# Performance work log

Hardware: AMD Instinct MI355X
Metric: run time of the kernel (lower is better)

The kernel has to match this reference:

```python
import jax, jax.numpy as jnp
import numpy as np

IMAGE_SIZE = 1024
DOWNSIZING = 64
THRESHOLD = 0.65  # default_threshold_target (threshold arg == 0)
NUM_BG_POINTS = 1
ORI_SHAPE = (2160, 3840)
EMBED_C, FEAT_H, FEAT_W = 256, 64, 64


def setup_inputs() -> dict:
    key = jax.random.key(0)
    k1, k2 = jax.random.split(key)
    image_embeddings = jax.random.normal(k1, (1, EMBED_C, FEAT_H, FEAT_W), dtype=jnp.float32)
    reference_feat = jax.random.normal(k2, (1, EMBED_C), dtype=jnp.float32) * 0.1
    ori_shape = jnp.array(ORI_SHAPE, dtype=jnp.int32)
    return {"image_embeddings": image_embeddings, "reference_feat": reference_feat, "ori_shape": ori_shape}


def _postprocess_masks(sim, H, W):
    # F.interpolate to (image_size, image_size), crop to pre-padded size, resize to ori_shape
    sim = jax.image.resize(sim, (1, 1, IMAGE_SIZE, IMAGE_SIZE), method="bilinear", antialias=False)
    scale = IMAGE_SIZE / max(H, W)
    ph = int(np.floor(H * scale + 0.5))
    pw = int(np.floor(W * scale + 0.5))
    sim = sim[..., :ph, :pw]
    return jax.image.resize(sim, (1, 1, H, W), method="bilinear", antialias=False)


def reference(image_embeddings, reference_feat, ori_shape):
    H, W = int(ori_shape[0]), int(ori_shape[1])
    # --- similarity map ---
    t = image_embeddings[0]                                   # (C, hf, wf)
    c, hf, wf = t.shape
    t = t / jnp.linalg.norm(t, axis=0, keepdims=True)         # channel-wise L2 norm
    sim = (reference_feat @ t.reshape(c, hf * wf)).reshape(1, 1, hf, wf)
    sim = _postprocess_masks(sim, H, W)
    m = sim[0, 0]                                             # (H, W)
    flat = m.reshape(-1)                                      # (H*W,)
    hw = H * W

    # --- background points: k smallest values ---
    _, bg_idx = jax.lax.top_k(-flat, NUM_BG_POINTS)
    bg_row = bg_idx // W
    bg_col = bg_idx % W
    bg_coords = jnp.stack([bg_col, bg_row], axis=1).astype(jnp.float32)  # (N, 2) = (x, y)

    # --- foreground points: grid-binned per-cell max (segment-max form of
    #     torch.where + unique + broadcast-equality + per-bin topk) ---
    ratio = IMAGE_SIZE / max(H, W)
    n_cells_side = IMAGE_SIZE // DOWNSIZING                    # 16; bounds grid rows/cols
    num_cells = n_cells_side * n_cells_side                    # 256 fixed
    idx = jnp.arange(hw, dtype=jnp.int32)
    ys = idx // W
    xs = idx % W
    gy = jnp.floor(ys * (ratio / DOWNSIZING)).astype(jnp.int32)
    gx = jnp.floor(xs * (ratio / DOWNSIZING)).astype(jnp.int32)
    seg = gy * n_cells_side + gx                               # grid id per pixel

    valid = flat > THRESHOLD
    masked = jnp.where(valid, flat, -jnp.inf)
    seg_max = jax.ops.segment_max(masked, seg, num_segments=num_cells)
    # first pixel achieving the cell max (matches torch.topk tie behavior)
    is_max = valid & (masked == seg_max[seg])
    cand = jnp.where(is_max, idx, hw)
    best = jax.ops.segment_min(cand, seg, num_segments=num_cells)
    cell_valid = best < hw
    bi = jnp.minimum(best, hw - 1)
    px = (bi % W).astype(jnp.float32)
    py = (bi // W).astype(jnp.float32)
    ps = flat[bi]
    points = jnp.stack([px, py, ps], axis=1)                   # (num_cells, 3) = (x, y, score)
    points = jnp.where(cell_valid[:, None], points, -1.0)      # mimic F.pad(value=-1) rows
    sort_key = jnp.where(cell_valid, ps, -jnp.inf)
    order = jnp.argsort(-sort_key)                             # score descending, invalid last
    points_scores = points[order]
    return points_scores, bg_coords
```

## Files before the change

### kernel.cpp

```cpp
#include <hip/hip_runtime.h>

#define W_OUT 3840
#define H_OUT 2160
#define IW 1024
#define IH 576
#define BAND 240

__device__ __forceinline__ unsigned int enc_f32(float f) {
    unsigned int b = __float_as_uint(f);
    return b ^ (0x80000000u | (unsigned int)((int)b >> 31));
}

__device__ __forceinline__ void release_vmem() {
    asm volatile("s_waitcnt vmcnt(0)" ::: "memory");
}

__global__ __launch_bounds__(256) void sim_kernel(
    const float* __restrict__ emb, const float* __restrict__ ref,
    float* __restrict__ sim,
    unsigned int* __restrict__ bandCnt,
    unsigned int* __restrict__ doneCnt)
{
    if (blockIdx.x == 0) {
        const int t = threadIdx.x;
        if (t < 9)          bandCnt[t * 16] = 0u;
        else if (t == 9)    *doneCnt = 0u;
    }
    const int lane = threadIdx.x & 63;
    const int wave = threadIdx.x >> 6;
    const int p = blockIdx.x * 64 + lane;
    const int cbase = wave * 64;
    float dot = 0.f, ss = 0.f;
#pragma unroll 8
    for (int cc = 0; cc < 64; ++cc) {
        int c = cbase + cc;
        float a = emb[c * 4096 + p];
        dot = fmaf(ref[c], a, dot);
        ss  = fmaf(a, a, ss);
    }
    __shared__ float sdot[4][64];
    __shared__ float sss[4][64];
    sdot[wave][lane] = dot;
    sss[wave][lane]  = ss;
    __syncthreads();
    if (wave == 0) {
        float d = (sdot[0][lane] + sdot[1][lane]) + (sdot[2][lane] + sdot[3][lane]);
        float s = (sss[0][lane] + sss[1][lane]) + (sss[2][lane] + sss[3][lane]);
        sim[p] = d / sqrtf(s);
    }
}

__global__ __launch_bounds__(256) void scan_kernel(
    const float* __restrict__ sim,
    unsigned long long* __restrict__ cellPart,
    unsigned long long* __restrict__ bgPart,
    unsigned long long* __restrict__ bandTab,
    unsigned long long* __restrict__ bgBand,
    unsigned int* __restrict__ bandCnt,
    unsigned int* __restrict__ doneCnt,
    float* __restrict__ out)
{
    __shared__ float4 I4[2][IW / 4];
    __shared__ unsigned long long wmin[4];
    __shared__ unsigned long long bred[16][17];
    __shared__ unsigned int lastFlag;
    __shared__ float sk[256];
    float* I0 = (float*)&I4[0][0];
    float* I1 = (float*)&I4[1][0];

    const float INV375 = (float)(1.0 / 3.75);
    const float INV16  = 0.0625f;

    const int y   = blockIdx.x;
    const int tid = threadIdx.x;
    const int band = y / BAND;

    float fy  = ((float)y + 0.5f) * INV375 - 0.5f;
    float fyf = floorf(fy);
    float wy  = fy - fyf;
    int ai = (int)fyf;
    int a1 = min(max(ai + 1, 0), IH - 1);
    int a0 = min(max(ai,     0), IH - 1);

    for (int r = 0; r < 2; ++r) {
        int a = (r == 0) ? a0 : a1;
        float fa  = ((float)a + 0.5f) * INV16 - 0.5f;
        float faf = floorf(fa);
        float wa  = fa - faf;
        int si = (int)faf;
        int s1 = min(max(si + 1, 0), 63);
        int s0 = min(max(si,     0), 63);
        const float* row0 = sim + s0 * 64;
        const float* row1 = sim + s1 * 64;
        float* dst = (r == 0) ? I0 : I1;
        for (int b = tid; b < IW; b += 256) {
            float fb  = ((float)b + 0.5f) * INV16 - 0.5f;
            float fbf = floorf(fb);
            float wb  = fb - fbf;
            int ci = (int)fbf;
            int c1 = min(max(ci + 1, 0), 63);
            int c0 = min(max(ci,     0), 63);
            float v0 = row0[c0] * (1.f - wb) + row0[c1] * wb;
            float v1 = row1[c0] * (1.f - wb) + row1[c1] * wb;
            dst[b] = v0 * (1.f - wa) + v1 * wa;
        }
    }
    __syncthreads();

    unsigned long long bestCell = 0ull;
    unsigned long long bestBg   = 0xFFFFFFFFFFFFFFFFull;
    const int x0 = tid * 15;
    const unsigned int idxBase = (unsigned int)(y * W_OUT + x0);

#define UPD(F, jj) {                                                        \
        unsigned long long top = ((unsigned long long)enc_f32(F)) << 32;    \
        unsigned int idx = idxBase + (jj);                                  \
        unsigned long long bgk = top | (unsigned long long)idx;             \
        unsigned long long ck  = top | (unsigned long long)(~idx);          \
        if (ck  > bestCell) bestCell = ck;                                  \
        if (bgk < bestBg)   bestBg   = bgk;                                 \
    }

    if (tid == 0 || tid == 255) {
#pragma unroll
        for (int j = 0; j < 15; ++j) {
            int x = x0 + j;
            float fx  = ((float)x + 0.5f) * INV375 - 0.5f;
            float fxf = floorf(fx);
            float wx  = fx - fxf;
            int bi = (int)fxf;
            int b1 = min(max(bi + 1, 0), IW - 1);
            int b0 = min(max(bi,     0), IW - 1);
            float v0 = I0[b0] * (1.f - wx) + I0[b1] * wx;
            float v1 = I1[b0] * (1.f - wx) + I1[b1] * wx;
            float F  = v0 * (1.f - wy) + v1 * wy;
            UPD(F, j)
        }
    } else {
        float4 A0 = I4[0][tid - 1], B0 = I4[0][tid], C0 = I4[0][tid + 1];
        float4 A1 = I4[1][tid - 1], B1 = I4[1][tid], C1 = I4[1][tid + 1];
        const float rr0[12] = {A0.x,A0.y,A0.z,A0.w, B0.x,B0.y,B0.z,B0.w, C0.x,C0.y,C0.z,C0.w};
        const float rr1[12] = {A1.x,A1.y,A1.z,A1.w, B1.x,B1.y,B1.z,B1.w, C1.x,C1.y,C1.z,C1.w};

#define PX(j, i0) {                                                         \
            float fx  = ((float)(x0 + (j)) + 0.5f) * INV375 - 0.5f;         \
            float fxf = floorf(fx);                                         \
            float wx  = fx - fxf;                                           \
            float v0 = rr0[(i0)] * (1.f - wx) + rr0[(i0) + 1] * wx;         \
            float v1 = rr1[(i0)] * (1.f - wx) + rr1[(i0) + 1] * wx;         \
            float F  = v0 * (1.f - wy) + v1 * wy;                           \
            UPD(F, j)                                                       \
        }
        PX(0,3)  PX(1,3)  PX(2,4)  PX(3,4)  PX(4,4)
        PX(5,4)  PX(6,5)  PX(7,5)  PX(8,5)  PX(9,6)
        PX(10,6) PX(11,6) PX(12,6) PX(13,7) PX(14,7)
#undef PX
    }
#undef UPD

#pragma unroll
    for (int m = 1; m <= 8; m <<= 1) {
        unsigned long long o = __shfl_xor(bestCell, m, 64);
        if (o > bestCell) bestCell = o;
    }
    if ((tid & 15) == 0)
        atomicExch(&cellPart[y * 16 + (tid >> 4)], bestCell);

#pragma unroll
    for (int m = 1; m <= 32; m <<= 1) {
        unsigned long long o = __shfl_xor(bestBg, m, 64);
        if (o < bestBg) bestBg = o;
    }
    if ((tid & 63) == 0) wmin[tid >> 6] = bestBg;
    __syncthreads();
    if (tid == 0) {
        unsigned long long b0 = wmin[0] < wmin[1] ? wmin[0] : wmin[1];
        unsigned long long b1 = wmin[2] < wmin[3] ? wmin[2] : wmin[3];
        atomicExch(&bgPart[y], b0 < b1 ? b0 : b1);
        release_vmem();
        unsigned int old = atomicAdd(&bandCnt[band * 16], 1u);
        lastFlag = (old == (unsigned int)(BAND - 1)) ? 1u : 0u;
    }
    __syncthreads();
    if (!lastFlag) return;

    {
        const int cx  = tid & 15;
        const int sub = tid >> 4;
        unsigned long long* src = cellPart + (band * BAND) * 16 + cx;
        unsigned long long mx = 0ull;
#pragma unroll
        for (int i = 0; i < 15; ++i) {
            unsigned long long v = atomicMax(&src[(sub * 15 + i) * 16], 0ull);
            if (v > mx) mx = v;
        }
        bred[sub][cx] = mx;

        unsigned long long bm = (tid < BAND)
            ? atomicMin(&bgPart[band * BAND + tid], 0xFFFFFFFFFFFFFFFFull)
            : 0xFFFFFFFFFFFFFFFFull;
#pragma unroll
        for (int m = 1; m <= 32; m <<= 1) {
            unsigned long long o = __shfl_xor(bm, m, 64);
            if (o < bm) bm = o;
        }
        if ((tid & 63) == 0) wmin[tid >> 6] = bm;
    }
    __syncthreads();
    if (tid < 16) {
        unsigned long long mx = bred[0][tid];
#pragma unroll
        for (int s = 1; s < 16; ++s) {
            unsigned long long v = bred[s][tid];
            if (v > mx) mx = v;
        }
        atomicExch(&bandTab[band * 16 + tid], mx);
    }
    if (tid == 0) {
        unsigned long long b0 = wmin[0] < wmin[1] ? wmin[0] : wmin[1];
        unsigned long long b1 = wmin[2] < wmin[3] ? wmin[2] : wmin[3];
        atomicExch(&bgBand[band], b0 < b1 ? b0 : b1);
    }
    __syncthreads();
    if (tid == 0) {
        release_vmem();
        unsigned int old = atomicAdd(doneCnt, 1u);
        lastFlag = (old == 8u) ? 1u : 0u;
    }
    __syncthreads();
    if (!lastFlag) return;

    float px = -1.f, py = -1.f, ps = -1.f;
    float key = -__builtin_huge_valf();
    if (tid < 144) {
        unsigned long long best = atomicMax(&bandTab[tid], 0ull);
        if (best != 0ull) {
            unsigned int e = (unsigned int)(best >> 32);
            unsigned int b = (e & 0x80000000u) ? (e ^ 0x80000000u) : ~e;
            float v = __uint_as_float(b);
            if (v > 0.65f) {
                unsigned int idx = ~((unsigned int)(best & 0xFFFFFFFFull));
                px = (float)(idx % W_OUT);
                py = (float)(idx / W_OUT);
                ps = v;
                key = v;
            }
        }
    }

    sk[tid] = key;
    __syncthreads();
    int rank = 0;
    for (int j = 0; j < 256; ++j) {
        float kj = sk[j];
        if (kj > key || (kj == key && j < tid)) rank++;
    }
    out[rank * 3 + 0] = px;
    out[rank * 3 + 1] = py;
    out[rank * 3 + 2] = ps;

    if (tid < 16) {
        unsigned long long b = (tid < 9) ? atomicMin(&bgBand[tid], 0xFFFFFFFFFFFFFFFFull)
                                         : 0xFFFFFFFFFFFFFFFFull;
#pragma unroll
        for (int m = 1; m <= 8; m <<= 1) {
            unsigned long long o = __shfl_xor(b, m, 64);
            if (o < b) b = o;
        }
        if (tid == 0) {
            unsigned int idx = (unsigned int)(b & 0xFFFFFFFFull);
            out[256 * 3 + 0] = (float)(idx % W_OUT);
            out[256 * 3 + 1] = (float)(idx / W_OUT);
        }
    }
}

extern "C" void kernel_launch(void* const* d_in, const int* in_sizes, int n_in,
                              void* d_out, int out_size, void* d_ws, size_t ws_size,
                              hipStream_t stream) {
    (void)in_sizes; (void)n_in; (void)out_size; (void)ws_size;
    const float* emb = (const float*)d_in[0];
    const float* ref = (const float*)d_in[1];
    float* out = (float*)d_out;

    char* ws = (char*)d_ws;
    float*              sim      = (float*)ws;
    unsigned long long* cellPart = (unsigned long long*)(ws + 16384);
    unsigned long long* bgPart   = (unsigned long long*)(ws + 292864);
    unsigned long long* bandTab  = (unsigned long long*)(ws + 310144);
    unsigned long long* bgBand   = (unsigned long long*)(ws + 311296);
    unsigned int*       bandCnt  = (unsigned int*)(ws + 311424);
    unsigned int*       doneCnt  = (unsigned int*)(ws + 312000);

    sim_kernel<<<64, 256, 0, stream>>>(emb, ref, sim, bandCnt, doneCnt);
    scan_kernel<<<H_OUT, 256, 0, stream>>>(sim, cellPart, bgPart, bandTab, bgBand,
                                           bandCnt, doneCnt, out);
}
```

Baseline: 91.12 us.

## Process four output rows per scan block sharing three intermediate rows

Each scan block now handles four consecutive output rows. It builds three vertically interpolated intermediate rows in shared memory once and reuses them across the four rows, instead of building two rows per output row. This cuts the block count, the per-block reduction and atomic traffic, and the band-finalisation work. The cost is fewer blocks for parallelism and longer serial work per block.

```diff
diff --git a/kernel.cpp b/kernel.cpp
--- a/kernel.cpp
+++ b/kernel.cpp
@@ -5,6 +5,9 @@
 #define IW 1024
 #define IH 576
 #define BAND 240
+#define RPB 4
+#define NBLK (H_OUT / RPB)
+#define BPB (BAND / RPB)
 
 __device__ __forceinline__ unsigned int enc_f32(float f) {
     unsigned int b = __float_as_uint(f);
@@ -60,49 +63,47 @@
     unsigned int* __restrict__ doneCnt,
     float* __restrict__ out)
 {
-    __shared__ float4 I4[2][IW / 4];
+    __shared__ float4 IC4[3][IW / 4];
     __shared__ unsigned long long wmin[4];
     __shared__ unsigned long long bred[16][17];
     __shared__ unsigned int lastFlag;
     __shared__ float sk[256];
-    float* I0 = (float*)&I4[0][0];
-    float* I1 = (float*)&I4[1][0];
 
     const float INV375 = (float)(1.0 / 3.75);
     const float INV16  = 0.0625f;
 
-    const int y   = blockIdx.x;
+    const int blk = blockIdx.x;
+    const int y0  = blk * RPB;
     const int tid = threadIdx.x;
-    const int band = y / BAND;
-
-    float fy  = ((float)y + 0.5f) * INV375 - 0.5f;
-    float fyf = floorf(fy);
-    float wy  = fy - fyf;
-    int ai = (int)fyf;
-    int a1 = min(max(ai + 1, 0), IH - 1);
-    int a0 = min(max(ai,     0), IH - 1);
-
-    for (int r = 0; r < 2; ++r) {
-        int a = (r == 0) ? a0 : a1;
-        float fa  = ((float)a + 0.5f) * INV16 - 0.5f;
-        float faf = floorf(fa);
-        float wa  = fa - faf;
-        int si = (int)faf;
-        int s1 = min(max(si + 1, 0), 63);
-        int s0 = min(max(si,     0), 63);
-        const float* row0 = sim + s0 * 64;
-        const float* row1 = sim + s1 * 64;
-        float* dst = (r == 0) ? I0 : I1;
-        for (int b = tid; b < IW; b += 256) {
-            float fb  = ((float)b + 0.5f) * INV16 - 0.5f;
-            float fbf = floorf(fb);
-            float wb  = fb - fbf;
-            int ci = (int)fbf;
-            int c1 = min(max(ci + 1, 0), 63);
-            int c0 = min(max(ci,     0), 63);
-            float v0 = row0[c0] * (1.f - wb) + row0[c1] * wb;
-            float v1 = row1[c0] * (1.f - wb) + row1[c1] * wb;
-            dst[b] = v0 * (1.f - wa) + v1 * wa;
+    const int band = y0 / BAND;
+
+    {
+        float fy0  = ((float)y0 + 0.5f) * INV375 - 0.5f;
+        int ai0 = (int)floorf(fy0);
+        int amin = min(max(ai0, 0), IH - 1);
+
+        for (int k = 0; k < 3; ++k) {
+            int a = amin + k;
+            float fa  = ((float)a + 0.5f) * INV16 - 0.5f;
+            float faf = floorf(fa);
+            float wa  = fa - faf;
+            int si = (int)faf;
+            int s1 = min(max(si + 1, 0), 63);
+            int s0 = min(max(si,     0), 63);
+            const float* row0 = sim + s0 * 64;
+            const float* row1 = sim + s1 * 64;
+            float* dst = (float*)&IC4[k][0];
+            for (int b = tid; b < IW; b += 256) {
+                float fb  = ((float)b + 0.5f) * INV16 - 0.5f;
+                float fbf = floorf(fb);
+                float wb  = fb - fbf;
+                int ci = (int)fbf;
+                int c1 = min(max(ci + 1, 0), 63);
+                int c0 = min(max(ci,     0), 63);
+                float v0 = row0[c0] * (1.f - wb) + row0[c1] * wb;
+                float v1 = row1[c0] * (1.f - wb) + row1[c1] * wb;
+                dst[b] = v0 * (1.f - wa) + v1 * wa;
+            }
         }
     }
     __syncthreads();
@@ -110,7 +111,12 @@
     unsigned long long bestCell = 0ull;
     unsigned long long bestBg   = 0xFFFFFFFFFFFFFFFFull;
     const int x0 = tid * 15;
-    const unsigned int idxBase = (unsigned int)(y * W_OUT + x0);
+
+    int amin;
+    {
+        float fy0 = ((float)y0 + 0.5f) * INV375 - 0.5f;
+        amin = min(max((int)floorf(fy0), 0), IH - 1);
+    }
 
 #define UPD(F, jj) {                                                        \
         unsigned long long top = ((unsigned long long)enc_f32(F)) << 32;    \
@@ -121,40 +127,56 @@
         if (bgk < bestBg)   bestBg   = bgk;                                 \
     }
 
-    if (tid == 0 || tid == 255) {
-#pragma unroll
-        for (int j = 0; j < 15; ++j) {
-            int x = x0 + j;
-            float fx  = ((float)x + 0.5f) * INV375 - 0.5f;
-            float fxf = floorf(fx);
-            float wx  = fx - fxf;
-            int bi = (int)fxf;
-            int b1 = min(max(bi + 1, 0), IW - 1);
-            int b0 = min(max(bi,     0), IW - 1);
-            float v0 = I0[b0] * (1.f - wx) + I0[b1] * wx;
-            float v1 = I1[b0] * (1.f - wx) + I1[b1] * wx;
-            float F  = v0 * (1.f - wy) + v1 * wy;
-            UPD(F, j)
-        }
-    } else {
-        float4 A0 = I4[0][tid - 1], B0 = I4[0][tid], C0 = I4[0][tid + 1];
-        float4 A1 = I4[1][tid - 1], B1 = I4[1][tid], C1 = I4[1][tid + 1];
-        const float rr0[12] = {A0.x,A0.y,A0.z,A0.w, B0.x,B0.y,B0.z,B0.w, C0.x,C0.y,C0.z,C0.w};
-        const float rr1[12] = {A1.x,A1.y,A1.z,A1.w, B1.x,B1.y,B1.z,B1.w, C1.x,C1.y,C1.z,C1.w};
-
-#define PX(j, i0) {                                                         \
+#pragma unroll 1
+    for (int jr = 0; jr < RPB; ++jr) {
+        const int y = y0 + jr;
+        float fy  = ((float)y + 0.5f) * INV375 - 0.5f;
+        float fyf = floorf(fy);
+        float wy  = fy - fyf;
+        int ai = (int)fyf;
+        int a1 = min(max(ai + 1, 0), IH - 1);
+        int a0 = min(max(ai,     0), IH - 1);
+        const int i0 = a0 - amin;
+        const int i1 = a1 - amin;
+        const float* I0 = (const float*)&IC4[i0][0];
+        const float* I1 = (const float*)&IC4[i1][0];
+        const unsigned int idxBase = (unsigned int)(y * W_OUT + x0);
+
+        if (tid == 0 || tid == 255) {
+#pragma unroll
+            for (int j = 0; j < 15; ++j) {
+                int x = x0 + j;
+                float fx  = ((float)x + 0.5f) * INV375 - 0.5f;
+                float fxf = floorf(fx);
+                float wx  = fx - fxf;
+                int bi = (int)fxf;
+                int b1 = min(max(bi + 1, 0), IW - 1);
+                int b0 = min(max(bi,     0), IW - 1);
+                float v0 = I0[b0] * (1.f - wx) + I0[b1] * wx;
+                float v1 = I1[b0] * (1.f - wx) + I1[b1] * wx;
+                float F  = v0 * (1.f - wy) + v1 * wy;
+                UPD(F, j)
+            }
+        } else {
+            float4 A0 = IC4[i0][tid - 1], B0 = IC4[i0][tid], C0 = IC4[i0][tid + 1];
+            float4 A1 = IC4[i1][tid - 1], B1 = IC4[i1][tid], C1 = IC4[i1][tid + 1];
+            const float rr0[12] = {A0.x,A0.y,A0.z,A0.w, B0.x,B0.y,B0.z,B0.w, C0.x,C0.y,C0.z,C0.w};
+            const float rr1[12] = {A1.x,A1.y,A1.z,A1.w, B1.x,B1.y,B1.z,B1.w, C1.x,C1.y,C1.z,C1.w};
+
+#define PX(j, i0w) {                                                        \
             float fx  = ((float)(x0 + (j)) + 0.5f) * INV375 - 0.5f;         \
             float fxf = floorf(fx);                                         \
             float wx  = fx - fxf;                                           \
-            float v0 = rr0[(i0)] * (1.f - wx) + rr0[(i0) + 1] * wx;         \
-            float v1 = rr1[(i0)] * (1.f - wx) + rr1[(i0) + 1] * wx;         \
+            float v0 = rr0[(i0w)] * (1.f - wx) + rr0[(i0w) + 1] * wx;       \
+            float v1 = rr1[(i0w)] * (1.f - wx) + rr1[(i0w) + 1] * wx;       \
             float F  = v0 * (1.f - wy) + v1 * wy;                           \
             UPD(F, j)                                                       \
         }
-        PX(0,3)  PX(1,3)  PX(2,4)  PX(3,4)  PX(4,4)
-        PX(5,4)  PX(6,5)  PX(7,5)  PX(8,5)  PX(9,6)
-        PX(10,6) PX(11,6) PX(12,6) PX(13,7) PX(14,7)
+            PX(0,3)  PX(1,3)  PX(2,4)  PX(3,4)  PX(4,4)
+            PX(5,4)  PX(6,5)  PX(7,5)  PX(8,5)  PX(9,6)
+            PX(10,6) PX(11,6) PX(12,6) PX(13,7) PX(14,7)
 #undef PX
+        }
     }
 #undef UPD
 
@@ -164,7 +186,7 @@
         if (o > bestCell) bestCell = o;
     }
     if ((tid & 15) == 0)
-        atomicExch(&cellPart[y * 16 + (tid >> 4)], bestCell);
+        atomicExch(&cellPart[blk * 16 + (tid >> 4)], bestCell);
 
 #pragma unroll
     for (int m = 1; m <= 32; m <<= 1) {
@@ -176,10 +198,10 @@
     if (tid == 0) {
         unsigned long long b0 = wmin[0] < wmin[1] ? wmin[0] : wmin[1];
         unsigned long long b1 = wmin[2] < wmin[3] ? wmin[2] : wmin[3];
-        atomicExch(&bgPart[y], b0 < b1 ? b0 : b1);
+        atomicExch(&bgPart[blk], b0 < b1 ? b0 : b1);
         release_vmem();
         unsigned int old = atomicAdd(&bandCnt[band * 16], 1u);
-        lastFlag = (old == (unsigned int)(BAND - 1)) ? 1u : 0u;
+        lastFlag = (old == (unsigned int)(BPB - 1)) ? 1u : 0u;
     }
     __syncthreads();
     if (!lastFlag) return;
@@ -187,17 +209,20 @@
     {
         const int cx  = tid & 15;
         const int sub = tid >> 4;
-        unsigned long long* src = cellPart + (band * BAND) * 16 + cx;
+        unsigned long long* src = cellPart + (band * BPB) * 16 + cx;
         unsigned long long mx = 0ull;
 #pragma unroll
-        for (int i = 0; i < 15; ++i) {
-            unsigned long long v = atomicMax(&src[(sub * 15 + i) * 16], 0ull);
-            if (v > mx) mx = v;
+        for (int i = 0; i < 4; ++i) {
+            int r = sub * 4 + i;
+            if (r < BPB) {
+                unsigned long long v = atomicMax(&src[r * 16], 0ull);
+                if (v > mx) mx = v;
+            }
         }
         bred[sub][cx] = mx;
 
-        unsigned long long bm = (tid < BAND)
-            ? atomicMin(&bgPart[band * BAND + tid], 0xFFFFFFFFFFFFFFFFull)
+        unsigned long long bm = (tid < BPB)
+            ? atomicMin(&bgPart[band * BPB + tid], 0xFFFFFFFFFFFFFFFFull)
             : 0xFFFFFFFFFFFFFFFFull;
 #pragma unroll
         for (int m = 1; m <= 32; m <<= 1) {
@@ -286,13 +311,13 @@
     char* ws = (char*)d_ws;
     float*              sim      = (float*)ws;
     unsigned long long* cellPart = (unsigned long long*)(ws + 16384);
-    unsigned long long* bgPart   = (unsigned long long*)(ws + 292864);
-    unsigned long long* bandTab  = (unsigned long long*)(ws + 310144);
-    unsigned long long* bgBand   = (unsigned long long*)(ws + 311296);
-    unsigned int*       bandCnt  = (unsigned int*)(ws + 311424);
-    unsigned int*       doneCnt  = (unsigned int*)(ws + 312000);
+    unsigned long long* bgPart   = (unsigned long long*)(ws + 85504);
+    unsigned long long* bandTab  = (unsigned long long*)(ws + 89824);
+    unsigned long long* bgBand   = (unsigned long long*)(ws + 90976);
+    unsigned int*       bandCnt  = (unsigned int*)(ws + 91136);
+    unsigned int*       doneCnt  = (unsigned int*)(ws + 91712);
 
     sim_kernel<<<64, 256, 0, stream>>>(emb, ref, sim, bandCnt, doneCnt);
-    scan_kernel<<<H_OUT, 256, 0, stream>>>(sim, cellPart, bgPart, bandTab, bgBand,
-                                           bandCnt, doneCnt, out);
-}
+    scan_kernel<<<NBLK, 256, 0, stream>>>(sim, cellPart, bgPart, bandTab, bgBand,
+                                          bandCnt, doneCnt, out);
+}
```

After: 87.82 us, median of 2. 1.04x faster.
